# Kernel tuning notes

Measured on AMD Instinct MI355X. Metric: run time of the kernel, lower is better.

## Reference

```python
import jax, jax.numpy as jnp
import numpy as np

N = 50000      # nodes
E = 800000     # edges (before self-loops)
F_IN = 128     # num_features
H = 4          # heads
C = 64         # hidden_channels
HC = H * C     # 256
NEG_SLOPE = 0.2


def setup_inputs() -> dict:
    key = jax.random.key(0)
    ks = jax.random.split(key, 20)
    x = jax.random.normal(ks[0], (N, F_IN), dtype=jnp.float32)
    edge_index = jax.random.randint(ks[1], (2, E), 0, N, dtype=jnp.int32)
    s = 0.05
    inp = {"x": x, "edge_index": edge_index}
    dims_in = [F_IN, HC, HC, HC]
    for l in range(4):
        kW, ka, kb = jax.random.split(ks[2 + l], 3)
        inp[f"W{l+1}"] = jax.random.normal(kW, (dims_in[l], HC), dtype=jnp.float32) * s
        inp[f"a_src{l+1}"] = jax.random.normal(ka, (H, C), dtype=jnp.float32) * s
        inp[f"a_dst{l+1}"] = jax.random.normal(kb, (H, C), dtype=jnp.float32) * s
        inp[f"b{l+1}"] = jnp.zeros((HC,), dtype=jnp.float32)
    return inp


def gat_conv(x, src, dst, W, a_src, a_dst, b):
    # x: [N, F_in] -> h: [N, H, C]
    h = (x @ W).reshape(N, H, C)
    es = jnp.sum(h * a_src, axis=-1)  # [N, H] per-node source logits
    ed = jnp.sum(h * a_dst, axis=-1)  # [N, H]
    e = jax.nn.leaky_relu(es[src] + ed[dst], NEG_SLOPE)  # [Etot, H]
    m = jax.ops.segment_max(e, dst, num_segments=N)      # per-dst max
    m = jnp.where(jnp.isfinite(m), m, 0.0)
    ex = jnp.exp(e - m[dst])
    denom = jax.ops.segment_sum(ex, dst, num_segments=N)
    alpha = ex / (denom[dst] + 1e-16)                     # edge softmax
    out = jax.ops.segment_sum(alpha[:, :, None] * h[src], dst, num_segments=N)
    return out.reshape(N, HC) + b


def reference(x, edge_index,
              W1, a_src1, a_dst1, b1,
              W2, a_src2, a_dst2, b2,
              W3, a_src3, a_dst3, b3,
              W4, a_src4, a_dst4, b4):
    loop = jnp.arange(N, dtype=edge_index.dtype)
    src = jnp.concatenate([edge_index[0], loop])  # add self-loops (PyG default)
    dst = jnp.concatenate([edge_index[1], loop])
    x1 = jax.nn.relu(gat_conv(x, src, dst, W1, a_src1, a_dst1, b1))
    x2 = jax.nn.relu(gat_conv(x1, src, dst, W2, a_src2, a_dst2, b2))
    x3 = jax.nn.relu(gat_conv(x2 + x1, src, dst, W3, a_src3, a_dst3, b3))
    x4 = jax.nn.relu(gat_conv(x2 + x3, src, dst, W4, a_src4, a_dst4, b4))
    # NOTE: source code calls conv4 again (not conv5) -- reproduced faithfully
    x5 = gat_conv(x4 + x3, src, dst, W4, a_src4, a_dst4, b4)
    return x5
```

## Files before the change

### kernel.cpp

```cpp
#include <hip/hip_runtime.h>
#include <hip/hip_bf16.h>

#define N_NODES 50000
#define E_EDGES 800000
#define ETOT (E_EDGES + N_NODES)
#define HC 256
#define NHEAD 4
#define CHAN 64
#define NEG 0.2f
#define NBLK ((N_NODES + 1023) / 1024)

typedef _Float16 half8 __attribute__((ext_vector_type(8)));
typedef _Float16 half4v __attribute__((ext_vector_type(4)));
typedef float float4v __attribute__((ext_vector_type(4)));


__global__ void count_kernel(const int* __restrict__ ei, int* __restrict__ counts) {
    int i = blockIdx.x * blockDim.x + threadIdx.x;
    if (i >= ETOT) return;
    int dst = (i < E_EDGES) ? ei[E_EDGES + i] : (i - E_EDGES);
    atomicAdd(&counts[dst], 1);
}

__global__ __launch_bounds__(256) void blocksum_kernel(const int* __restrict__ counts,
                                                       int* __restrict__ blocksums) {
    __shared__ int s[4];
    int b = blockIdx.x, tid = threadIdx.x;
    int base = b * 1024;
    int sum = 0;
    #pragma unroll
    for (int r = 0; r < 4; ++r) {
        int idx = base + r * 256 + tid;
        sum += (idx < N_NODES) ? counts[idx] : 0;
    }
    #pragma unroll
    for (int m = 1; m < 64; m <<= 1) sum += __shfl_xor(sum, m, 64);
    if ((tid & 63) == 0) s[tid >> 6] = sum;
    __syncthreads();
    if (tid == 0) blocksums[b] = s[0] + s[1] + s[2] + s[3];
}

__global__ __launch_bounds__(64) void blockscan_kernel(int* __restrict__ blocksums) {
    int tid = threadIdx.x;
    int v = (tid < NBLK) ? blocksums[tid] : 0;
    #pragma unroll
    for (int off = 1; off < 64; off <<= 1) {
        int t = __shfl_up(v, off, 64);
        if (tid >= off) v += t;
    }
    if (tid < NBLK) blocksums[tid] = v;
}

__global__ __launch_bounds__(1024) void scatter_scan_kernel(const int* __restrict__ counts,
                                                            const int* __restrict__ blocksums,
                                                            int* __restrict__ offsets,
                                                            int* __restrict__ cursor) {
    __shared__ int s[1024];
    int b = blockIdx.x, tid = threadIdx.x;
    int idx = b * 1024 + tid;
    int v = (idx < N_NODES) ? counts[idx] : 0;
    s[tid] = v;
    __syncthreads();
    for (int off = 1; off < 1024; off <<= 1) {
        int t = (tid >= off) ? s[tid - off] : 0;
        __syncthreads();
        s[tid] += t;
        __syncthreads();
    }
    int excl = s[tid] - v + (b > 0 ? blocksums[b - 1] : 0);
    if (idx < N_NODES) { offsets[idx] = excl; cursor[idx] = excl; }
    if (idx == N_NODES - 1) offsets[N_NODES] = excl + v;
}

__global__ void fill_kernel(const int* __restrict__ ei, int* __restrict__ cursor,
                            int* __restrict__ csr_src) {
    int i = blockIdx.x * blockDim.x + threadIdx.x;
    if (i >= ETOT) return;
    int src, dst;
    if (i < E_EDGES) { src = ei[i]; dst = ei[E_EDGES + i]; }
    else             { src = i - E_EDGES; dst = src; }
    int pos = atomicAdd(&cursor[dst], 1);
    csr_src[pos] = src;
}


__global__ void wsplit_kernel(const float* __restrict__ W, _Float16* __restrict__ Wth,
                              _Float16* __restrict__ Wtl, int K) {
    int id = blockIdx.x * 256 + threadIdx.x;
    if (id >= K * 256) return;
    int n = id & 255, k = id >> 8;
    float w = W[(size_t)k * 256 + n];
    _Float16 h = (_Float16)w;
    _Float16 l = (_Float16)(w - (float)h);
    Wth[(size_t)n * K + k] = h;
    Wtl[(size_t)n * K + k] = l;
}

__global__ void xsplit_kernel(const float* __restrict__ x, _Float16* __restrict__ xh,
                              _Float16* __restrict__ xl, int total) {
    int id = blockIdx.x * 256 + threadIdx.x;
    if (id >= total) return;
    float v = x[id];
    _Float16 h = (_Float16)v;
    xh[id] = h;
    xl[id] = (_Float16)(v - (float)h);
}


#define LDK 40

__global__ __launch_bounds__(256) void gemm_mfma_kernel(
        const _Float16* __restrict__ A1h, const _Float16* __restrict__ A1l,
        const _Float16* __restrict__ A2h,
        const _Float16* __restrict__ Wth, const _Float16* __restrict__ Wtl,
        const float* __restrict__ a_src, const float* __restrict__ a_dst,
        _Float16* __restrict__ H16, float* __restrict__ es, float* __restrict__ ed,
        int M, int K) {
    __shared__ _Float16 Ah[64][LDK];
    __shared__ _Float16 Al[64][LDK];
    __shared__ _Float16 Bh[256][LDK];
    __shared__ _Float16 Bl[256][LDK];

    int tid = threadIdx.x;
    int m0 = blockIdx.x * 64;
    int w = tid >> 6, lane = tid & 63;
    int rn = w * 64;
    int fr = lane & 15;
    int q  = lane >> 4;
    int fk = q * 8;

    int wr = tid >> 2;
    int wk = (tid & 3) * 8;

    bool has_lo = (A1l != nullptr);
    bool has2   = (A2h != nullptr);

    float4v acc[4][4];
    #pragma unroll
    for (int i = 0; i < 4; ++i)
        #pragma unroll
        for (int j = 0; j < 4; ++j)
            acc[i][j] = (float4v){0.f, 0.f, 0.f, 0.f};

    half8 pa, pal, pbh[4], pbl[4];

    auto load_tile = [&](int k0) {
        int row = m0 + wr;
        pa  = (half8)(_Float16)0;
        pal = (half8)(_Float16)0;
        if (row < M) {
            pa = *(const half8*)(A1h + (size_t)row * K + k0 + wk);
            if (has2) {
                half8 u = *(const half8*)(A2h + (size_t)row * K + k0 + wk);
                pa = pa + u;
            }
            if (has_lo) pal = *(const half8*)(A1l + (size_t)row * K + k0 + wk);
        }
        #pragma unroll
        for (int g = 0; g < 4; ++g) {
            int r = g * 64 + wr;
            pbh[g] = *(const half8*)(Wth + (size_t)r * K + k0 + wk);
            pbl[g] = *(const half8*)(Wtl + (size_t)r * K + k0 + wk);
        }
    };

    load_tile(0);
    for (int k0 = 0; k0 < K; k0 += 32) {
        *(half8*)&Ah[wr][wk] = pa;
        if (has_lo) *(half8*)&Al[wr][wk] = pal;
        #pragma unroll
        for (int g = 0; g < 4; ++g) {
            int r = g * 64 + wr;
            *(half8*)&Bh[r][wk] = pbh[g];
            *(half8*)&Bl[r][wk] = pbl[g];
        }
        __syncthreads();
        if (k0 + 32 < K) load_tile(k0 + 32);
        half8 afh[4], bfh[4], bfl[4];
        #pragma unroll
        for (int t = 0; t < 4; ++t) {
            afh[t] = *(const half8*)&Ah[t * 16 + fr][fk];
            bfh[t] = *(const half8*)&Bh[rn + t * 16 + fr][fk];
            bfl[t] = *(const half8*)&Bl[rn + t * 16 + fr][fk];
        }
        if (has_lo) {
            half8 afl[4];
            #pragma unroll
            for (int t = 0; t < 4; ++t) afl[t] = *(const half8*)&Al[t * 16 + fr][fk];
            #pragma unroll
            for (int tm = 0; tm < 4; ++tm)
                #pragma unroll
                for (int tn = 0; tn < 4; ++tn)
                    acc[tm][tn] = __builtin_amdgcn_mfma_f32_16x16x32_f16(
                        afl[tm], bfh[tn], acc[tm][tn], 0, 0, 0);
        }
        #pragma unroll
        for (int tm = 0; tm < 4; ++tm)
            #pragma unroll
            for (int tn = 0; tn < 4; ++tn) {
                float4v c = acc[tm][tn];
                c = __builtin_amdgcn_mfma_f32_16x16x32_f16(afh[tm], bfl[tn], c, 0, 0, 0);
                c = __builtin_amdgcn_mfma_f32_16x16x32_f16(afh[tm], bfh[tn], c, 0, 0, 0);
                acc[tm][tn] = c;
            }
        __syncthreads();
    }

    float asv[4], adv[4];
    #pragma unroll
    for (int tn = 0; tn < 4; ++tn) {
        asv[tn] = a_src[w * CHAN + tn * 16 + fr];
        adv[tn] = a_dst[w * CHAN + tn * 16 + fr];
    }
    #pragma unroll
    for (int tm = 0; tm < 4; ++tm) {
        #pragma unroll
        for (int i = 0; i < 4; ++i) {
            int row = m0 + tm * 16 + q * 4 + i;
            float ps = 0.f, pd = 0.f;
            #pragma unroll
            for (int tn = 0; tn < 4; ++tn) {
                float hv = acc[tm][tn][i];
                ps += hv * asv[tn];
                pd += hv * adv[tn];
                if (row < M)
                    H16[(size_t)row * HC + rn + tn * 16 + fr] = (_Float16)hv;
            }
            #pragma unroll
            for (int msk = 1; msk < 16; msk <<= 1) {
                ps += __shfl_xor(ps, msk, 64);
                pd += __shfl_xor(pd, msk, 64);
            }
            if (fr == 0 && row < M) {
                es[row * NHEAD + w] = ps;
                ed[row * NHEAD + w] = pd;
            }
        }
    }
}


__global__ __launch_bounds__(256) void gat_aggregate_kernel(
        const _Float16* __restrict__ H16, const float* __restrict__ es, const float* __restrict__ ed,
        const int* __restrict__ offsets, const int* __restrict__ csr_src,
        const float* __restrict__ bias, _Float16* __restrict__ out16,
        float* __restrict__ out32, int do_relu) {
    __shared__ float alpha_lds[4][256];
    int tid = threadIdx.x;
    int w = tid >> 6, lane = tid & 63;
    int n = blockIdx.x * 4 + w;
    int off = offsets[n];
    int deg = offsets[n + 1] - off;
    float4 edv = *(const float4*)(ed + (size_t)n * 4);

    if (deg <= 64) {
        int sreg = 0;
        float4 e4 = make_float4(-1e30f, -1e30f, -1e30f, -1e30f);
        if (lane < deg) {
            sreg = csr_src[off + lane];
            float4 esv = *(const float4*)(es + (size_t)sreg * 4);
            e4.x = esv.x + edv.x; e4.y = esv.y + edv.y;
            e4.z = esv.z + edv.z; e4.w = esv.w + edv.w;
            e4.x = (e4.x > 0.f) ? e4.x : NEG * e4.x;
            e4.y = (e4.y > 0.f) ? e4.y : NEG * e4.y;
            e4.z = (e4.z > 0.f) ? e4.z : NEG * e4.z;
            e4.w = (e4.w > 0.f) ? e4.w : NEG * e4.w;
        }
        float4 m4 = e4;
        #pragma unroll
        for (int msk = 1; msk < 64; msk <<= 1) {
            m4.x = fmaxf(m4.x, __shfl_xor(m4.x, msk, 64));
            m4.y = fmaxf(m4.y, __shfl_xor(m4.y, msk, 64));
            m4.z = fmaxf(m4.z, __shfl_xor(m4.z, msk, 64));
            m4.w = fmaxf(m4.w, __shfl_xor(m4.w, msk, 64));
        }
        float4 ex4 = make_float4(0.f, 0.f, 0.f, 0.f);
        if (lane < deg) {
            ex4.x = __expf(e4.x - m4.x); ex4.y = __expf(e4.y - m4.y);
            ex4.z = __expf(e4.z - m4.z); ex4.w = __expf(e4.w - m4.w);
        }
        float4 l4 = ex4;
        #pragma unroll
        for (int msk = 1; msk < 64; msk <<= 1) {
            l4.x += __shfl_xor(l4.x, msk, 64);
            l4.y += __shfl_xor(l4.y, msk, 64);
            l4.z += __shfl_xor(l4.z, msk, 64);
            l4.w += __shfl_xor(l4.w, msk, 64);
        }
        float4 a4;
        a4.x = ex4.x / (l4.x + 1e-16f);
        a4.y = ex4.y / (l4.y + 1e-16f);
        a4.z = ex4.z / (l4.z + 1e-16f);
        a4.w = ex4.w / (l4.w + 1e-16f);
        *(float4*)&alpha_lds[w][lane * 4] = a4;

        int hl = lane & 31, side = lane >> 5;
        int hd = hl >> 3;
        float av[8] = {0.f, 0.f, 0.f, 0.f, 0.f, 0.f, 0.f, 0.f};
        #pragma unroll 2
        for (int j = side; j < deg; j += 2) {
            int s = __shfl(sreg, j, 64);
            float al = alpha_lds[w][j * 4 + hd];
            half8 hv = *(const half8*)(H16 + (size_t)s * HC + hl * 8);
            #pragma unroll
            for (int c = 0; c < 8; ++c) av[c] += al * (float)hv[c];
        }
        #pragma unroll
        for (int c = 0; c < 8; ++c) av[c] += __shfl_xor(av[c], 32, 64);
        if (side == 0) {
            float4 b0 = *(const float4*)(bias + hl * 8);
            float4 b1 = *(const float4*)(bias + hl * 8 + 4);
            float o[8] = {av[0] + b0.x, av[1] + b0.y, av[2] + b0.z, av[3] + b0.w,
                          av[4] + b1.x, av[5] + b1.y, av[6] + b1.z, av[7] + b1.w};
            if (do_relu)
                #pragma unroll
                for (int c = 0; c < 8; ++c) o[c] = fmaxf(o[c], 0.f);
            if (out16) {
                half8 ov = {(_Float16)o[0], (_Float16)o[1], (_Float16)o[2], (_Float16)o[3],
                            (_Float16)o[4], (_Float16)o[5], (_Float16)o[6], (_Float16)o[7]};
                *(half8*)(out16 + (size_t)n * HC + hl * 8) = ov;
            } else {
                *(float4*)(out32 + (size_t)n * HC + hl * 8) =
                    make_float4(o[0], o[1], o[2], o[3]);
                *(float4*)(out32 + (size_t)n * HC + hl * 8 + 4) =
                    make_float4(o[4], o[5], o[6], o[7]);
            }
        }
        return;
    }

    int head = lane >> 4;
    float4 acc0 = make_float4(0.f, 0.f, 0.f, 0.f);
    float m[4] = {-1e30f, -1e30f, -1e30f, -1e30f};
    float l[4] = {0.f, 0.f, 0.f, 0.f};
    for (int base = 0; base < deg; base += 64) {
        int j = base + lane;
        if (j < deg) {
            int s = csr_src[off + j];
            float4 esv = *(const float4*)(es + (size_t)s * 4);
            float e[4] = {esv.x + edv.x, esv.y + edv.y, esv.z + edv.z, esv.w + edv.w};
            #pragma unroll
            for (int h = 0; h < 4; ++h) {
                e[h] = (e[h] > 0.f) ? e[h] : NEG * e[h];
                float M2 = fmaxf(m[h], e[h]);
                l[h] = l[h] * __expf(m[h] - M2) + __expf(e[h] - M2);
                m[h] = M2;
            }
        }
    }
    #pragma unroll
    for (int msk = 1; msk < 64; msk <<= 1) {
        #pragma unroll
        for (int h = 0; h < 4; ++h) {
            float mo = __shfl_xor(m[h], msk, 64);
            float lo = __shfl_xor(l[h], msk, 64);
            float M2 = fmaxf(m[h], mo);
            l[h] = l[h] * __expf(m[h] - M2) + lo * __expf(mo - M2);
            m[h] = M2;
        }
    }
    float fm = m[head];
    float fr2 = 1.f / (l[head] + 1e-16f);
    float edh = ((const float*)&edv)[head];
    for (int j = 0; j < deg; ++j) {
        int s = csr_src[off + j];
        float e = es[(size_t)s * 4 + head] + edh;
        e = (e > 0.f) ? e : NEG * e;
        float alpha = __expf(e - fm) * fr2;
        half4v h0 = *(const half4v*)(H16 + (size_t)s * HC + lane * 4);
        acc0.x += alpha * (float)h0[0]; acc0.y += alpha * (float)h0[1];
        acc0.z += alpha * (float)h0[2]; acc0.w += alpha * (float)h0[3];
    }
    float4 b4 = *(const float4*)(bias + lane * 4);
    float o[4] = {acc0.x + b4.x, acc0.y + b4.y, acc0.z + b4.z, acc0.w + b4.w};
    if (do_relu)
        #pragma unroll
        for (int c = 0; c < 4; ++c) o[c] = fmaxf(o[c], 0.f);
    if (out16) {
        half4v ov = {(_Float16)o[0], (_Float16)o[1], (_Float16)o[2], (_Float16)o[3]};
        *(half4v*)(out16 + (size_t)n * HC + lane * 4) = ov;
    } else {
        *(float4*)(out32 + (size_t)n * HC + lane * 4) = make_float4(o[0], o[1], o[2], o[3]);
    }
}


extern "C" void kernel_launch(void* const* d_in, const int* in_sizes, int n_in,
                              void* d_out, int out_size, void* d_ws, size_t ws_size,
                              hipStream_t stream) {
    const float* x  = (const float*)d_in[0];
    const int*   ei = (const int*)d_in[1];
    const float *W[5], *Asrc[5], *Adst[5], *Bs[5];
    for (int l = 0; l < 4; ++l) {
        W[l]    = (const float*)d_in[2 + l * 4];
        Asrc[l] = (const float*)d_in[3 + l * 4];
        Adst[l] = (const float*)d_in[4 + l * 4];
        Bs[l]   = (const float*)d_in[5 + l * 4];
    }
    W[4] = W[3]; Asrc[4] = Asrc[3]; Adst[4] = Adst[3]; Bs[4] = Bs[3];

    char* ws = (char*)d_ws;
    size_t off = 0;
    auto alloc = [&](size_t bytes) -> void* {
        void* p = ws + off;
        off += (bytes + 255) & ~(size_t)255;
        return p;
    };
    _Float16* h16  = (_Float16*)alloc((size_t)N_NODES * HC * 2);
    _Float16* xa   = (_Float16*)alloc((size_t)N_NODES * HC * 2);
    _Float16* xb   = (_Float16*)alloc((size_t)N_NODES * HC * 2);
    _Float16* xc   = (_Float16*)alloc((size_t)N_NODES * HC * 2);
    _Float16* xd   = (_Float16*)alloc((size_t)N_NODES * HC * 2);
    _Float16* xh   = (_Float16*)alloc((size_t)N_NODES * 128 * 2);
    _Float16* xl   = (_Float16*)alloc((size_t)N_NODES * 128 * 2);
    float* es      = (float*)alloc((size_t)N_NODES * 4 * 4);
    float* ed      = (float*)alloc((size_t)N_NODES * 4 * 4);
    int*   counts  = (int*)alloc((size_t)N_NODES * 4);
    int*   offsets = (int*)alloc((size_t)(N_NODES + 1) * 4);
    int*   cursor  = (int*)alloc((size_t)N_NODES * 4);
    int*   csr_src = (int*)alloc((size_t)ETOT * 4);
    int*   blocksums = (int*)alloc((size_t)NBLK * 4);
    _Float16 *Wth[5], *Wtl[5];
    int Ks[4] = {128, 256, 256, 256};
    for (int l = 0; l < 4; ++l) {
        Wth[l] = (_Float16*)alloc((size_t)256 * Ks[l] * 2);
        Wtl[l] = (_Float16*)alloc((size_t)256 * Ks[l] * 2);
    }
    Wth[4] = Wth[3]; Wtl[4] = Wtl[3];

    hipMemsetAsync(counts, 0, (size_t)N_NODES * 4, stream);
    count_kernel<<<(ETOT + 255) / 256, 256, 0, stream>>>(ei, counts);
    blocksum_kernel<<<NBLK, 256, 0, stream>>>(counts, blocksums);
    blockscan_kernel<<<1, 64, 0, stream>>>(blocksums);
    scatter_scan_kernel<<<NBLK, 1024, 0, stream>>>(counts, blocksums, offsets, cursor);
    fill_kernel<<<(ETOT + 255) / 256, 256, 0, stream>>>(ei, cursor, csr_src);
    for (int l = 0; l < 4; ++l)
        wsplit_kernel<<<(Ks[l] * 256 + 255) / 256, 256, 0, stream>>>(W[l], Wth[l], Wtl[l], Ks[l]);
    xsplit_kernel<<<(N_NODES * 128 + 255) / 256, 256, 0, stream>>>(x, xh, xl, N_NODES * 128);

    auto layer = [&](const _Float16* a1h, const _Float16* a1l, const _Float16* a2h,
                     int K, int l, _Float16* o16, float* o32, int relu) {
        gemm_mfma_kernel<<<(N_NODES + 63) / 64, 256, 0, stream>>>(
            a1h, a1l, a2h, Wth[l], Wtl[l], Asrc[l], Adst[l], h16, es, ed, N_NODES, K);
        gat_aggregate_kernel<<<N_NODES / 4, 256, 0, stream>>>(
            h16, es, ed, offsets, csr_src, Bs[l], o16, o32, relu);
    };

    float* out = (float*)d_out;
    layer(xh, xl,      nullptr, 128, 0, xa, nullptr, 1);
    layer(xa, nullptr, nullptr, 256, 1, xb, nullptr, 1);
    layer(xb, nullptr, xa,      256, 2, xc, nullptr, 1);
    layer(xb, nullptr, xc,      256, 3, xd, nullptr, 1);
    layer(xd, nullptr, xc,      256, 4, nullptr, out, 0);
}
```

Baseline: 840.8 us.

## Drop max-subtraction in small-degree softmax and defer normalization to output

```diff
diff --git a/kernel.cpp b/kernel.cpp
--- a/kernel.cpp
+++ b/kernel.cpp
@@ -245,7 +245,8 @@
         const int* __restrict__ offsets, const int* __restrict__ csr_src,
         const float* __restrict__ bias, _Float16* __restrict__ out16,
         float* __restrict__ out32, int do_relu) {
-    __shared__ float alpha_lds[4][256];
+    __shared__ float ex_lds[4][256];
+    __shared__ int   src_lds[4][64];
     int tid = threadIdx.x;
     int w = tid >> 6, lane = tid & 63;
     int n = blockIdx.x * 4 + w;
@@ -254,31 +255,52 @@
     float4 edv = *(const float4*)(ed + (size_t)n * 4);
 
     if (deg <= 64) {
-        int sreg = 0;
-        float4 e4 = make_float4(-1e30f, -1e30f, -1e30f, -1e30f);
+        int sreg = n;
+        float4 ex4 = make_float4(0.f, 0.f, 0.f, 0.f);
         if (lane < deg) {
             sreg = csr_src[off + lane];
             float4 esv = *(const float4*)(es + (size_t)sreg * 4);
+            float4 e4;
             e4.x = esv.x + edv.x; e4.y = esv.y + edv.y;
             e4.z = esv.z + edv.z; e4.w = esv.w + edv.w;
             e4.x = (e4.x > 0.f) ? e4.x : NEG * e4.x;
             e4.y = (e4.y > 0.f) ? e4.y : NEG * e4.y;
             e4.z = (e4.z > 0.f) ? e4.z : NEG * e4.z;
             e4.w = (e4.w > 0.f) ? e4.w : NEG * e4.w;
-        }
-        float4 m4 = e4;
-        #pragma unroll
-        for (int msk = 1; msk < 64; msk <<= 1) {
-            m4.x = fmaxf(m4.x, __shfl_xor(m4.x, msk, 64));
-            m4.y = fmaxf(m4.y, __shfl_xor(m4.y, msk, 64));
-            m4.z = fmaxf(m4.z, __shfl_xor(m4.z, msk, 64));
-            m4.w = fmaxf(m4.w, __shfl_xor(m4.w, msk, 64));
-        }
-        float4 ex4 = make_float4(0.f, 0.f, 0.f, 0.f);
-        if (lane < deg) {
-            ex4.x = __expf(e4.x - m4.x); ex4.y = __expf(e4.y - m4.y);
-            ex4.z = __expf(e4.z - m4.z); ex4.w = __expf(e4.w - m4.w);
-        }
+            ex4.x = __expf(e4.x); ex4.y = __expf(e4.y);
+            ex4.z = __expf(e4.z); ex4.w = __expf(e4.w);
+        }
+        src_lds[w][lane] = sreg;
+        *(float4*)&ex_lds[w][lane * 4] = ex4;
+
+        int hl = lane & 31, side = lane >> 5;
+        int hd = hl >> 3;
+        float av[8] = {0.f, 0.f, 0.f, 0.f, 0.f, 0.f, 0.f, 0.f};
+        int degr = (deg + 7) & ~7;
+        #pragma unroll 2
+        for (int j0 = 0; j0 < degr; j0 += 8) {
+            int j = j0 + side;
+            int s0 = src_lds[w][j];
+            int s1 = src_lds[w][j + 2];
+            int s2 = src_lds[w][j + 4];
+            int s3 = src_lds[w][j + 6];
+            float w0 = ex_lds[w][j * 4 + hd];
+            float w1 = ex_lds[w][(j + 2) * 4 + hd];
+            float w2 = ex_lds[w][(j + 4) * 4 + hd];
+            float w3 = ex_lds[w][(j + 6) * 4 + hd];
+            half8 h0 = *(const half8*)(H16 + (size_t)s0 * HC + hl * 8);
+            half8 h1 = *(const half8*)(H16 + (size_t)s1 * HC + hl * 8);
+            half8 h2 = *(const half8*)(H16 + (size_t)s2 * HC + hl * 8);
+            half8 h3 = *(const half8*)(H16 + (size_t)s3 * HC + hl * 8);
+            #pragma unroll
+            for (int c = 0; c < 8; ++c) {
+                av[c] += w0 * (float)h0[c];
+                av[c] += w1 * (float)h1[c];
+                av[c] += w2 * (float)h2[c];
+                av[c] += w3 * (float)h3[c];
+            }
+        }
+
         float4 l4 = ex4;
         #pragma unroll
         for (int msk = 1; msk < 64; msk <<= 1) {
@@ -287,31 +309,17 @@
             l4.z += __shfl_xor(l4.z, msk, 64);
             l4.w += __shfl_xor(l4.w, msk, 64);
         }
-        float4 a4;
-        a4.x = ex4.x / (l4.x + 1e-16f);
-        a4.y = ex4.y / (l4.y + 1e-16f);
-        a4.z = ex4.z / (l4.z + 1e-16f);
-        a4.w = ex4.w / (l4.w + 1e-16f);
-        *(float4*)&alpha_lds[w][lane * 4] = a4;
-
-        int hl = lane & 31, side = lane >> 5;
-        int hd = hl >> 3;
-        float av[8] = {0.f, 0.f, 0.f, 0.f, 0.f, 0.f, 0.f, 0.f};
-        #pragma unroll 2
-        for (int j = side; j < deg; j += 2) {
-            int s = __shfl(sreg, j, 64);
-            float al = alpha_lds[w][j * 4 + hd];
-            half8 hv = *(const half8*)(H16 + (size_t)s * HC + hl * 8);
-            #pragma unroll
-            for (int c = 0; c < 8; ++c) av[c] += al * (float)hv[c];
-        }
         #pragma unroll
         for (int c = 0; c < 8; ++c) av[c] += __shfl_xor(av[c], 32, 64);
         if (side == 0) {
+            float denom = (hd == 0) ? l4.x : (hd == 1) ? l4.y : (hd == 2) ? l4.z : l4.w;
+            float scale = 1.f / (denom + 1e-16f);
             float4 b0 = *(const float4*)(bias + hl * 8);
             float4 b1 = *(const float4*)(bias + hl * 8 + 4);
-            float o[8] = {av[0] + b0.x, av[1] + b0.y, av[2] + b0.z, av[3] + b0.w,
-                          av[4] + b1.x, av[5] + b1.y, av[6] + b1.z, av[7] + b1.w};
+            float o[8] = {av[0] * scale + b0.x, av[1] * scale + b0.y,
+                          av[2] * scale + b0.z, av[3] * scale + b0.w,
+                          av[4] * scale + b1.x, av[5] * scale + b1.y,
+                          av[6] * scale + b1.z, av[7] * scale + b1.w};
             if (do_relu)
                 #pragma unroll
                 for (int c = 0; c < 8; ++c) o[c] = fmaxf(o[c], 0.f);
```

Measured after the change: 792.2 us. 1.06x faster.
